# Kernel optimization log

Hardware: AMD Instinct MI355X
Metric: run time of the kernel (lower is better)

## Reference

```python
import jax, jax.numpy as jnp
import numpy as np

B, T, D = 256, 128, 1024
H = 128          # lstm_hidden
CF = 128         # conv_filters
K = 9            # num_labels
CE_W = 0.2
EPS = 1e-5


def conv1d(x, w, b, pad):
    # x: (B, C, T), w: (O, I, k)
    y = jax.lax.conv_general_dilated(x, w, (1,), [(pad, pad)],
                                     dimension_numbers=('NCH', 'OIH', 'NCH'))
    return y + b[None, :, None]


def batchnorm(x, g, beta):
    # training-mode BN over (N, W) per channel, biased variance (torch default)
    m = x.mean(axis=(0, 2), keepdims=True)
    v = x.var(axis=(0, 2), keepdims=True)
    return (x - m) * jax.lax.rsqrt(v + EPS) * g[None, :, None] + beta[None, :, None]


def lstm_dir(x, Wih, Whh, bih, bhh, reverse):
    # x: (B, T, D_in). PyTorch gate order: i, f, g, o.
    xg = jnp.einsum('btd,gd->btg', x, Wih) + bih + bhh  # (B, T, 4H)
    h0 = jnp.zeros((x.shape[0], Whh.shape[1]), x.dtype)
    c0 = jnp.zeros_like(h0)

    def step(carry, g_t):
        h, c = carry
        gates = g_t + h @ Whh.T
        i, f, g, o = jnp.split(gates, 4, axis=-1)
        c = jax.nn.sigmoid(f) * c + jax.nn.sigmoid(i) * jnp.tanh(g)
        h = jax.nn.sigmoid(o) * jnp.tanh(c)
        return (h, c), h

    _, hs = jax.lax.scan(step, (h0, c0), jnp.swapaxes(xg, 0, 1), reverse=reverse)
    return jnp.swapaxes(hs, 0, 1)  # (B, T, H)


def crf_log_partition(em, mask, start, trans, end):
    # em: (B, T, K), mask: (B, T) bool (mask[:,0] assumed True)
    score = start[None, :] + em[:, 0]  # (B, K)

    def step(score, inp):
        em_t, m_t = inp  # (B, K), (B,)
        nxt = jax.nn.logsumexp(score[:, :, None] + trans[None] + em_t[:, None, :], axis=1)
        return jnp.where(m_t[:, None], nxt, score), None

    score, _ = jax.lax.scan(step, score,
                            (jnp.swapaxes(em[:, 1:], 0, 1), jnp.swapaxes(mask[:, 1:], 0, 1)))
    return jax.nn.logsumexp(score + end[None, :], axis=1)  # (B,)


def crf_numerator(em, tags, mask, start, trans, end):
    mf = mask.astype(em.dtype)
    em_sc = jnp.take_along_axis(em, tags[..., None], axis=-1)[..., 0]  # (B, T)
    tr_sc = trans[tags[:, :-1], tags[:, 1:]]                           # (B, T-1)
    seq_ends = mask.astype(jnp.int32).sum(axis=1) - 1
    last_tags = jnp.take_along_axis(tags, seq_ends[:, None], axis=1)[:, 0]
    return (start[tags[:, 0]] + em_sc[:, 0]
            + ((tr_sc + em_sc[:, 1:]) * mf[:, 1:]).sum(axis=1)
            + end[last_tags])


def setup_inputs() -> dict:
    key = jax.random.key(0)
    ks = jax.random.split(key, 32)
    s = 0.05
    inp = {
        'embeddings': jax.random.normal(ks[0], (B, T, D), jnp.float32),
        'attention_mask': jnp.ones((B, T), jnp.int32),
        'labels': jax.random.randint(ks[1], (B, T), 0, K).astype(jnp.int64),
        'conv5_w': jax.random.normal(ks[2], (CF, D, 5)) * s,
        'conv5_b': jnp.zeros((CF,)),
        'bn1_g': jnp.ones((CF,)),
        'bn1_b': jnp.zeros((CF,)),
        'Wih_f': jax.random.normal(ks[3], (4 * H, CF)) * s,
        'Whh_f': jax.random.normal(ks[4], (4 * H, H)) * s,
        'bih_f': jnp.zeros((4 * H,)),
        'bhh_f': jnp.zeros((4 * H,)),
        'Wih_b': jax.random.normal(ks[5], (4 * H, CF)) * s,
        'Whh_b': jax.random.normal(ks[6], (4 * H, H)) * s,
        'bih_b': jnp.zeros((4 * H,)),
        'bhh_b': jnp.zeros((4 * H,)),
        'conv7_w': jax.random.normal(ks[7], (CF, 2 * H, 7)) * s,
        'conv7_b': jnp.zeros((CF,)),
        'conv9_w': jax.random.normal(ks[8], (CF, 2 * H, 9)) * s,
        'conv9_b': jnp.zeros((CF,)),
        'bn2_g': jnp.ones((2 * CF,)),
        'bn2_b': jnp.zeros((2 * CF,)),
        'cls_w': jax.random.normal(ks[9], (K, 2 * CF)) * s,
        'cls_b': jnp.zeros((K,)),
        'crf_start': jax.random.normal(ks[10], (K,)) * 0.1,
        'crf_trans': jax.random.normal(ks[11], (K, K)) * 0.1,
        'crf_end': jax.random.normal(ks[12], (K,)) * 0.1,
        'class_weights': jax.random.uniform(ks[13], (K,)) + 0.5,
    }
    return inp


def reference(embeddings, attention_mask, labels, conv5_w, conv5_b, bn1_g, bn1_b,
              Wih_f, Whh_f, bih_f, bhh_f, Wih_b, Whh_b, bih_b, bhh_b,
              conv7_w, conv7_b, conv9_w, conv9_b, bn2_g, bn2_b, cls_w, cls_b,
              crf_start, crf_trans, crf_end, class_weights):
    x = embeddings.astype(jnp.float32)
    xt = jnp.swapaxes(x, 1, 2)  # (B, D, T)
    xc = jax.nn.gelu(batchnorm(conv1d(xt, conv5_w, conv5_b, 2), bn1_g, bn1_b),
                     approximate=False)
    xl = jnp.swapaxes(xc, 1, 2)  # (B, T, CF)
    hf = lstm_dir(xl, Wih_f, Whh_f, bih_f, bhh_f, reverse=False)
    hb = lstm_dir(xl, Wih_b, Whh_b, bih_b, bhh_b, reverse=True)
    lstm_out = jnp.swapaxes(jnp.concatenate([hf, hb], axis=-1), 1, 2)  # (B, 2H, T)
    c7 = conv1d(lstm_out, conv7_w, conv7_b, 3)
    c9 = conv1d(lstm_out, conv9_w, conv9_b, 4)
    feat = jax.nn.gelu(batchnorm(jnp.concatenate([c7, c9], axis=1), bn2_g, bn2_b),
                       approximate=False)
    feat = jnp.swapaxes(feat, 1, 2)  # (B, T, 2CF); dropout p=0 -> identity
    logits = jnp.einsum('btf,kf->btk', feat, cls_w) + cls_b  # (B, T, K)

    mask = (attention_mask != 0) & (labels != -100)
    mod_labels = jnp.where(labels == -100, 0, labels).astype(jnp.int32)

    num = crf_numerator(logits, mod_labels, mask, crf_start, crf_trans, crf_end)
    logZ = crf_log_partition(logits, mask, crf_start, crf_trans, crf_end)
    crf_loss = -(num - logZ).mean()

    logp = jax.nn.log_softmax(logits, axis=-1).reshape(-1, K)
    y = labels.reshape(-1)
    valid = y != -100
    yi = jnp.where(valid, y, 0).astype(jnp.int32)
    nll = -jnp.take_along_axis(logp, yi[:, None], axis=1)[:, 0]
    w = jnp.where(valid, class_weights[yi], 0.0)
    ce_loss = (w * nll).sum() / w.sum()

    return (1.0 - CE_W) * crf_loss + CE_W * ce_loss
```

## Files before the change

kernel.cpp:

```cpp
#include <hip/hip_runtime.h>
#include <hip/hip_bf16.h>
#include <math.h>

#define BB 256
#define TT 128
#define DD 1024
#define CFF 128
#define HH 128
#define G4 512
#define NK 9

typedef __attribute__((ext_vector_type(8))) short bf16x8;
typedef __attribute__((ext_vector_type(4))) float f32x4;

__device__ __forceinline__ float bf_lo(unsigned u){ union{unsigned u; float f;} v; v.u = u << 16; return v.f; }
__device__ __forceinline__ float bf_hi(unsigned u){ union{unsigned u; float f;} v; v.u = u & 0xffff0000u; return v.f; }
__device__ __forceinline__ unsigned f2bf(float x){
    union{float f; unsigned u;} v; v.f = x;
    unsigned r = v.u + 0x7fffu + ((v.u >> 16) & 1u);
    return r >> 16;
}
__device__ __forceinline__ float fsig_fast(float x){
    return __builtin_amdgcn_rcpf(1.0f + __builtin_amdgcn_exp2f(-1.44269504f * x));
}
__device__ __forceinline__ float ftanh_fast(float x){
    return 1.0f - 2.0f * __builtin_amdgcn_rcpf(1.0f + __builtin_amdgcn_exp2f(2.88539008f * x));
}
__device__ __forceinline__ float gelu_exact(float x){
    return 0.5f*x*(1.0f + erff(x*0.70710678118654752440f));
}

__global__ __launch_bounds__(256) void prep_convw_kernel(
    const float* __restrict__ w, ushort* __restrict__ Wk, int CIN, int KS, int total)
{
    int i = blockIdx.x*256 + threadIdx.x;
    if (i >= total) return;
    int k = i % KS;
    int d = (i / KS) % CIN;
    int f = i / (KS * CIN);
    Wk[((size_t)(k*128 + f))*CIN + d] = (ushort)f2bf(w[i]);
}

__global__ __launch_bounds__(256) void prep_xg_kernel(
    const float* __restrict__ Wf, const float* __restrict__ Wb,
    const float* __restrict__ bif, const float* __restrict__ bhf,
    const float* __restrict__ bib, const float* __restrict__ bhb,
    ushort* __restrict__ Wxg, float* __restrict__ bias_xg)
{
    int i = blockIdx.x*256 + threadIdx.x;
    if (i < 65536) Wxg[i] = (ushort)f2bf(Wf[i]);
    else if (i < 131072) Wxg[i] = (ushort)f2bf(Wb[i - 65536]);
    else {
        int j = i - 131072;
        if (j < 512) bias_xg[j] = bif[j] + bhf[j];
        else if (j < 1024) bias_xg[j] = bib[j-512] + bhb[j-512];
    }
}

template<int CIN, int KS, int KSE_MAX, int SPLIT, bool IN_F32, bool OUT_BF16, bool XGT = false>
__global__ __launch_bounds__(256, 1) void conv_mfma_kernel(
    const void* __restrict__ in_v,
    const ushort* __restrict__ Wk_g,
    const float* __restrict__ bias_g,
    void* __restrict__ outA_v, void* __restrict__ outB_v,
    int OS, int co)
{
    constexpr int PAD = KS / 2;
    constexpr int ROWS = 128 + 2 * PAD;
    constexpr int NSTEP = (SPLIT == 1) ? (CIN / 64) : (CIN / 32);
    constexpr int ATOT = IN_F32 ? ROWS * 8 : ROWS * 4;
    constexpr int BTOT = KSE_MAX * 128 * 4;
    constexpr int AIT = (ATOT + 255) / 256;
    constexpr int BIT = (BTOT + 255) / 256;

    __shared__ ushort A_lds[ROWS * 32];
    __shared__ ushort B_lds[KSE_MAX * 128 * 32];

    const int tid = threadIdx.x;
    const int b   = blockIdx.x;
    const int by  = blockIdx.y;
    const int z   = blockIdx.z;
    const int dbase = (SPLIT == 1) ? z * (CIN / 2) : 0;
    const int k0    = (SPLIT == 2) ? z * KSE_MAX : 0;
    const int kse   = (SPLIT == 2) ? ((z == 0) ? KSE_MAX : (KS - KSE_MAX)) : KS;
    const ushort* __restrict__ Wk = Wk_g + (size_t)by * (size_t)(128 * CIN);
    const float* __restrict__ bias = bias_g + by * 128;

    float4 aRf[AIT];
    int4   aRb[AIT];
    int4   bR[BIT];

    auto stage_load = [&](int s) {
        const int d0 = dbase + s * 32;
        if constexpr (IN_F32) {
            const float* __restrict__ inp = (const float*)in_v;
#pragma unroll
            for (int it = 0; it < AIT; ++it) {
                int i = tid + it * 256;
                float4 v = make_float4(0.f, 0.f, 0.f, 0.f);
                if (i < ATOT) {
                    int r = i >> 3, c = i & 7;
                    int t = r - PAD;
                    if (t >= 0 && t < TT)
                        v = *reinterpret_cast<const float4*>(&inp[((size_t)b * TT + t) * CIN + d0 + c * 4]);
                }
                aRf[it] = v;
            }
        } else {
            const ushort* __restrict__ inp = (const ushort*)in_v;
#pragma unroll
            for (int it = 0; it < AIT; ++it) {
                int i = tid + it * 256;
                int4 v = make_int4(0, 0, 0, 0);
                if (i < ATOT) {
                    int r = i >> 2, c = i & 3;
                    int t = r - PAD;
                    if (t >= 0 && t < TT)
                        v = *reinterpret_cast<const int4*>(&inp[((size_t)b * TT + t) * CIN + d0 + c * 8]);
                }
                aRb[it] = v;
            }
        }
#pragma unroll
        for (int it = 0; it < BIT; ++it) {
            int i = tid + it * 256;
            int kk = i >> 9;
            int rem = i & 511;
            int f = rem >> 2, c = rem & 3;
            int4 v = make_int4(0, 0, 0, 0);
            if (kk < kse)
                v = *reinterpret_cast<const int4*>(&Wk[((size_t)((k0 + kk) * 128 + f)) * CIN + d0 + c * 8]);
            bR[it] = v;
        }
    };

    auto stage_write = [&]() {
        if constexpr (IN_F32) {
#pragma unroll
            for (int it = 0; it < AIT; ++it) {
                int i = tid + it * 256;
                if (i < ATOT) {
                    int r = i >> 3, c = i & 7;
                    float4 v = aRf[it];
                    ushort4 h;
                    h.x = (ushort)f2bf(v.x); h.y = (ushort)f2bf(v.y);
                    h.z = (ushort)f2bf(v.z); h.w = (ushort)f2bf(v.w);
                    int slot = (c >> 1) ^ (r & 3);
                    *reinterpret_cast<ushort4*>(&A_lds[r * 32 + slot * 8 + (c & 1) * 4]) = h;
                }
            }
        } else {
#pragma unroll
            for (int it = 0; it < AIT; ++it) {
                int i = tid + it * 256;
                if (i < ATOT) {
                    int r = i >> 2, c = i & 3;
                    int slot = c ^ (r & 3);
                    *reinterpret_cast<int4*>(&A_lds[r * 32 + slot * 8]) = aRb[it];
                }
            }
        }
#pragma unroll
        for (int it = 0; it < BIT; ++it) {
            int i = tid + it * 256;
            int kk = i >> 9;
            int rem = i & 511;
            int f = rem >> 2, c = rem & 3;
            int slot = c ^ (f & 3);
            *reinterpret_cast<int4*>(&B_lds[(kk * 128 + f) * 32 + slot * 8]) = bR[it];
        }
    };

    const int lane = tid & 63;
    const int wave = tid >> 6;
    const int lr = lane & 15;
    const int lk = lane >> 4;
    const int wm = wave >> 1;
    const int wn = wave & 1;

    f32x4 acc[4][4];
#pragma unroll
    for (int m = 0; m < 4; ++m)
#pragma unroll
        for (int n = 0; n < 4; ++n)
            acc[m][n] = (f32x4){0.f, 0.f, 0.f, 0.f};

    stage_load(0);
    stage_write();
    asm volatile("s_waitcnt lgkmcnt(0)" ::: "memory");
    __builtin_amdgcn_s_barrier();
    __builtin_amdgcn_sched_barrier(0);

    for (int s = 0; s < NSTEP; ++s) {
        if (s + 1 < NSTEP) stage_load(s + 1);
#pragma unroll
        for (int kk = 0; kk < KSE_MAX; ++kk) {
            bf16x8 af[4], bfr[4];
#pragma unroll
            for (int m = 0; m < 4; ++m) {
                int R = wm * 64 + m * 16 + lr + k0 + kk;
                if (kk >= kse) R = 0;
                af[m] = *reinterpret_cast<const bf16x8*>(&A_lds[R * 32 + ((lk ^ (R & 3)) * 8)]);
            }
#pragma unroll
            for (int n = 0; n < 4; ++n) {
                int Rb = kk * 128 + wn * 64 + n * 16 + lr;
                bfr[n] = *reinterpret_cast<const bf16x8*>(&B_lds[Rb * 32 + ((lk ^ (lr & 3)) * 8)]);
            }
#pragma unroll
            for (int m = 0; m < 4; ++m)
#pragma unroll
                for (int n = 0; n < 4; ++n)
                    acc[m][n] = __builtin_amdgcn_mfma_f32_16x16x32_bf16(af[m], bfr[n], acc[m][n], 0, 0, 0);
        }
        if (s + 1 < NSTEP) {
            asm volatile("s_waitcnt lgkmcnt(0)" ::: "memory");
            __builtin_amdgcn_s_barrier();
            __builtin_amdgcn_sched_barrier(0);
            stage_write();
            asm volatile("s_waitcnt lgkmcnt(0)" ::: "memory");
            __builtin_amdgcn_s_barrier();
            __builtin_amdgcn_sched_barrier(0);
        }
    }

    const bool addb = (SPLIT == 0) || (z == 0);
    void* out_v = (SPLIT != 0 && z == 1) ? outB_v : outA_v;
    float bv[4];
#pragma unroll
    for (int n = 0; n < 4; ++n) bv[n] = addb ? bias[wn * 64 + n * 16 + lr] : 0.f;
#pragma unroll
    for (int m = 0; m < 4; ++m) {
#pragma unroll
        for (int n = 0; n < 4; ++n) {
            int f = wn * 64 + n * 16 + lr;
#pragma unroll
            for (int q = 0; q < 4; ++q) {
                int trow = wm * 64 + m * 16 + lk * 4 + q;
                float val = acc[m][n][q] + bv[n];
                size_t idx;
                if constexpr (XGT) {
                    int dirg = by >> 2;
                    int g = by & 3;
                    idx = (size_t)dirg * 16777216u + (size_t)trow * 131072u
                        + (size_t)b * 512u + (size_t)(g * 128 + f);
                } else {
                    idx = ((size_t)b * TT + trow) * (size_t)OS + co + f;
                }
                if constexpr (OUT_BF16)
                    ((ushort*)out_v)[idx] = (ushort)f2bf(val);
                else
                    ((float*)out_v)[idx] = val;
            }
        }
    }
}

__global__ __launch_bounds__(256) void bn_stats_kernel(
    const float* __restrict__ y, const float* __restrict__ y2, int C, int rows_per_blk,
    float* __restrict__ sum, float* __restrict__ sqsum)
{
    int tpc = 256 / C;
    int c = threadIdx.x & (C - 1);
    int sub = threadIdx.x / C;
    size_t r0 = (size_t)blockIdx.x * rows_per_blk;
    float s = 0.f, s2 = 0.f;
    for (int r = sub; r < rows_per_blk; r += tpc) {
        size_t i = (r0 + r)*C + c;
        float v = y[i] + y2[i];
        s += v; s2 += v*v;
    }
    __shared__ float ls[256], ls2[256];
    ls[threadIdx.x] = s; ls2[threadIdx.x] = s2;
    __syncthreads();
    if (sub == 0) {
        for (int k = 1; k < tpc; ++k) { s += ls[c + k*C]; s2 += ls2[c + k*C]; }
        atomicAdd(&sum[c], s);
        atomicAdd(&sqsum[c], s2);
    }
}

__global__ __launch_bounds__(256) void bn_gelu_kernel(
    float* __restrict__ y, const float* __restrict__ y2, int Cmask,
    const float* __restrict__ sum, const float* __restrict__ sqsum,
    const float* __restrict__ g, const float* __restrict__ beta, float inv_n)
{
    size_t i = (size_t)blockIdx.x*256 + threadIdx.x;
    int c = (int)(i & (size_t)Cmask);
    float m = sum[c] * inv_n;
    float var = fmaxf(sqsum[c]*inv_n - m*m, 0.f);
    float xv = (y[i] + y2[i] - m) * rsqrtf(var + 1e-5f) * g[c] + beta[c];
    y[i] = gelu_exact(xv);
}

__global__ __launch_bounds__(512, 1) void lstm_mfma_kernel(
    const ushort* __restrict__ xg2,
    const float* __restrict__ Whhf, const float* __restrict__ Whhb,
    ushort* __restrict__ hfb)
{
    const int tid = threadIdx.x;
    const int lane = tid & 63;
    const int w = tid >> 6;
    const int jc = lane & 15;
    const int kq = lane >> 4;
    const int dir = blockIdx.x >> 4;
    const int b0 = (blockIdx.x & 15) << 4;
    const float* __restrict__ Whh = dir ? Whhb : Whhf;

    bf16x8 Wf[4][4];
#pragma unroll
    for (int g = 0; g < 4; ++g) {
        const float* wr = &Whh[(size_t)((g << 7) + (w << 4) + jc) * HH + (kq << 3)];
#pragma unroll
        for (int s = 0; s < 4; ++s) {
            float4 v0 = *reinterpret_cast<const float4*>(wr + (s << 5));
            float4 v1 = *reinterpret_cast<const float4*>(wr + (s << 5) + 4);
            union { bf16x8 v; ushort u[8]; } pk;
            pk.u[0] = (ushort)f2bf(v0.x); pk.u[1] = (ushort)f2bf(v0.y);
            pk.u[2] = (ushort)f2bf(v0.z); pk.u[3] = (ushort)f2bf(v0.w);
            pk.u[4] = (ushort)f2bf(v1.x); pk.u[5] = (ushort)f2bf(v1.y);
            pk.u[6] = (ushort)f2bf(v1.z); pk.u[7] = (ushort)f2bf(v1.w);
            Wf[g][s] = pk.v;
        }
    }

    __shared__ ushort h_lds[2][16 * 136];
    for (int i = tid; i < 16 * 136; i += 512) h_lds[0][i] = 0;
    f32x4 creg = (f32x4){0.f, 0.f, 0.f, 0.f};

    const ushort* __restrict__ xb = xg2 + (size_t)dir * 16777216u
        + (size_t)(b0 + jc) * 512u + (size_t)((w << 4) + (kq << 2));

    uint2 xA[4], xB[4];
    {
        int tt0 = dir ? (TT - 1) : 0;
        int tt1 = dir ? (TT - 2) : 1;
#pragma unroll
        for (int g = 0; g < 4; ++g) {
            xA[g] = *reinterpret_cast<const uint2*>(xb + (size_t)tt0 * 131072u + (g << 7));
            xB[g] = *reinterpret_cast<const uint2*>(xb + (size_t)tt1 * 131072u + (g << 7));
        }
    }

    __syncthreads();

    int cur = 0;
    const int hrd = jc * 136 + (kq << 3);
    const int col0 = (w << 4) + (kq << 2);

    auto step = [&](int t, uint2 (&xr)[4]) {
        const int tt_c = dir ? (TT - 1 - t) : t;
        f32x4 acc[4];
#pragma unroll
        for (int g = 0; g < 4; ++g) {
            acc[g][0] = bf_lo(xr[g].x);
            acc[g][1] = bf_hi(xr[g].x);
            acc[g][2] = bf_lo(xr[g].y);
            acc[g][3] = bf_hi(xr[g].y);
        }
        {
            int t2 = t + 2; if (t2 >= TT) t2 = TT - 1;
            int ttn = dir ? (TT - 1 - t2) : t2;
#pragma unroll
            for (int g = 0; g < 4; ++g)
                xr[g] = *reinterpret_cast<const uint2*>(xb + (size_t)ttn * 131072u + (g << 7));
        }
        bf16x8 Hf[4];
#pragma unroll
        for (int s = 0; s < 4; ++s)
            Hf[s] = *reinterpret_cast<const bf16x8*>(&h_lds[cur][hrd + (s << 5)]);
#pragma unroll
        for (int s = 0; s < 4; ++s)
#pragma unroll
            for (int g = 0; g < 4; ++g)
                acc[g] = __builtin_amdgcn_mfma_f32_16x16x32_bf16(Wf[g][s], Hf[s], acc[g], 0, 0, 0);
        float hv[4];
#pragma unroll
        for (int r = 0; r < 4; ++r) {
            float iv = fsig_fast(acc[0][r]);
            float fv = fsig_fast(acc[1][r]);
            float gv = ftanh_fast(acc[2][r]);
            float ov = fsig_fast(acc[3][r]);
            float c = fv * creg[r] + iv * gv;
            creg[r] = c;
            hv[r] = ov * ftanh_fast(c);
        }
        ushort4 hb;
        hb.x = (ushort)f2bf(hv[0]); hb.y = (ushort)f2bf(hv[1]);
        hb.z = (ushort)f2bf(hv[2]); hb.w = (ushort)f2bf(hv[3]);
        const int nxt = cur ^ 1;
        *reinterpret_cast<ushort4*>(&h_lds[nxt][jc * 136 + col0]) = hb;
        *reinterpret_cast<ushort4*>(&hfb[((size_t)(b0 + jc) * TT + tt_c) * 256 + (dir << 7) + col0]) = hb;
        asm volatile("s_waitcnt lgkmcnt(0)" ::: "memory");
        __builtin_amdgcn_s_barrier();
        __builtin_amdgcn_sched_barrier(0);
        cur = nxt;
    };

    for (int t = 0; t < TT; t += 2) {
        step(t, xA);
        step(t + 1, xB);
    }
}

__global__ __launch_bounds__(256) void logits_kernel(
    const float* __restrict__ feat, const float* __restrict__ cw,
    const float* __restrict__ cb, float* __restrict__ lg)
{
    __shared__ float wls[NK*256];
    for (int i = threadIdx.x; i < NK*256; i += 256) wls[i] = cw[i];
    __syncthreads();
    size_t row = (size_t)blockIdx.x*256 + threadIdx.x;
    const float* fr = &feat[row*256];
    float acc[NK];
#pragma unroll
    for (int k = 0; k < NK; ++k) acc[k] = 0.f;
    for (int c = 0; c < 256; c += 4) {
        float4 v = *reinterpret_cast<const float4*>(&fr[c]);
#pragma unroll
        for (int k = 0; k < NK; ++k)
            acc[k] += v.x*wls[k*256 + c] + v.y*wls[k*256 + c + 1]
                    + v.z*wls[k*256 + c + 2] + v.w*wls[k*256 + c + 3];
    }
#pragma unroll
    for (int k = 0; k < NK; ++k) lg[row*NK + k] = acc[k] + cb[k];
}

__global__ __launch_bounds__(256) void ce_kernel(
    const float* __restrict__ lg, const int* __restrict__ labels,
    const float* __restrict__ cw, float* __restrict__ acc2)
{
    size_t i = (size_t)blockIdx.x*256 + threadIdx.x;
    const float* l = &lg[i*NK];
    float mx = -1e30f;
#pragma unroll
    for (int k = 0; k < NK; ++k) mx = fmaxf(mx, l[k]);
    float se = 0.f;
#pragma unroll
    for (int k = 0; k < NK; ++k) se += expf(l[k] - mx);
    float lz = mx + logf(se);
    int y = labels[i];
    bool valid = (y != -100);
    int yi = valid ? y : 0;
    float nll = lz - l[yi];
    float wv = valid ? cw[yi] : 0.f;
    __shared__ float s1[256], s2[256];
    s1[threadIdx.x] = wv*nll;
    s2[threadIdx.x] = wv;
    __syncthreads();
    for (int s = 128; s > 0; s >>= 1) {
        if (threadIdx.x < s) { s1[threadIdx.x] += s1[threadIdx.x + s]; s2[threadIdx.x] += s2[threadIdx.x + s]; }
        __syncthreads();
    }
    if (threadIdx.x == 0) { atomicAdd(&acc2[0], s1[0]); atomicAdd(&acc2[1], s2[0]); }
}

__global__ __launch_bounds__(64) void crf_kernel(
    const float* __restrict__ lg, const int* __restrict__ att,
    const int* __restrict__ labels, const float* __restrict__ startv,
    const float* __restrict__ trans, const float* __restrict__ endv,
    float* __restrict__ numo, float* __restrict__ logzo)
{
    int b = blockIdx.x;
    int lane = threadIdx.x;
    int lane_c = (lane < NK) ? lane : 0;
    const float* em = &lg[(size_t)b*TT*NK];
    float tr[NK];
#pragma unroll
    for (int i = 0; i < NK; ++i) tr[i] = trans[i*NK + lane_c];
    float score = startv[lane_c] + em[lane_c];

    for (int t = 1; t < TT; ++t) {
        int lt = labels[b*TT + t];
        bool m = (att[b*TT + t] != 0) && (lt != -100);
        float vals[NK];
#pragma unroll
        for (int i = 0; i < NK; ++i)
            vals[i] = __shfl(score, i, 64) + tr[i];
        if (m) {
            float mx = vals[0];
#pragma unroll
            for (int i = 1; i < NK; ++i) mx = fmaxf(mx, vals[i]);
            float sm = 0.f;
#pragma unroll
            for (int i = 0; i < NK; ++i) sm += expf(vals[i] - mx);
            score = mx + logf(sm) + em[t*NK + lane_c];
        }
    }
    float fin = (lane < NK) ? (score + endv[lane_c]) : -1e30f;
    float mx = -1e30f;
#pragma unroll
    for (int i = 0; i < NK; ++i) mx = fmaxf(mx, __shfl(fin, i, 64));
    float sm = 0.f;
#pragma unroll
    for (int i = 0; i < NK; ++i) sm += expf(__shfl(fin, i, 64) - mx);
    if (lane == 0) logzo[b] = mx + logf(sm);

    if (lane == 0) {
        int l0 = labels[b*TT];
        int tag0 = (l0 == -100) ? 0 : l0;
        bool m0 = (att[b*TT] != 0) && (l0 != -100);
        float num = startv[tag0] + em[tag0];
        int prev = tag0;
        int cnt = m0 ? 1 : 0;
        for (int t = 1; t < TT; ++t) {
            int lt = labels[b*TT + t];
            bool m = (att[b*TT + t] != 0) && (lt != -100);
            int tag = (lt == -100) ? 0 : lt;
            if (m) { num += trans[prev*NK + tag] + em[t*NK + tag]; cnt++; }
            prev = tag;
        }
        int le = cnt - 1; if (le < 0) le = 0; if (le >= TT) le = TT - 1;
        int ll = labels[b*TT + le];
        int ltag = (ll == -100) ? 0 : ll;
        num += endv[ltag];
        numo[b] = num;
    }
}

__global__ __launch_bounds__(256) void finalize_kernel(
    const float* __restrict__ numo, const float* __restrict__ logzo,
    const float* __restrict__ acc2, float* __restrict__ out)
{
    __shared__ float red[256];
    int tid = threadIdx.x;
    red[tid] = numo[tid] - logzo[tid];
    __syncthreads();
    for (int s = 128; s > 0; s >>= 1) {
        if (tid < s) red[tid] += red[tid + s];
        __syncthreads();
    }
    if (tid == 0) {
        float crf = -(red[0] / (float)BB);
        float ce = acc2[0] / acc2[1];
        out[0] = 0.8f*crf + 0.2f*ce;
    }
}

extern "C" void kernel_launch(void* const* d_in, const int* in_sizes, int n_in,
                              void* d_out, int out_size, void* d_ws, size_t ws_size,
                              hipStream_t stream)
{
    const float* emb   = (const float*)d_in[0];
    const int*   att   = (const int*)  d_in[1];
    const int*   lab   = (const int*)  d_in[2];
    const float* c5w   = (const float*)d_in[3];
    const float* c5b   = (const float*)d_in[4];
    const float* bn1g  = (const float*)d_in[5];
    const float* bn1b  = (const float*)d_in[6];
    const float* Wihf  = (const float*)d_in[7];
    const float* Whhf  = (const float*)d_in[8];
    const float* bihf  = (const float*)d_in[9];
    const float* bhhf  = (const float*)d_in[10];
    const float* Wihb  = (const float*)d_in[11];
    const float* Whhb  = (const float*)d_in[12];
    const float* bihb  = (const float*)d_in[13];
    const float* bhhb  = (const float*)d_in[14];
    const float* c7w   = (const float*)d_in[15];
    const float* c7b   = (const float*)d_in[16];
    const float* c9w   = (const float*)d_in[17];
    const float* c9b   = (const float*)d_in[18];
    const float* bn2g  = (const float*)d_in[19];
    const float* bn2b  = (const float*)d_in[20];
    const float* clsw  = (const float*)d_in[21];
    const float* clsb  = (const float*)d_in[22];
    const float* cstart= (const float*)d_in[23];
    const float* ctrans= (const float*)d_in[24];
    const float* cend  = (const float*)d_in[25];
    const float* cwts  = (const float*)d_in[26];
    (void)in_sizes; (void)n_in; (void)out_size; (void)ws_size;

    char* wsb = (char*)d_ws;
    size_t off = 0;
    auto alloc = [&](size_t bytes) { void* p = wsb + off; off += (bytes + 255) & ~(size_t)255; return p; };
    float*  y1      = (float*) alloc((size_t)4194304*4);
    ushort* xg      = (ushort*)alloc((size_t)2*16777216*2);
    ushort* hfb     = (ushort*)alloc((size_t)8388608*2);
    float*  lg      = (float*) alloc((size_t)294912*4);
    ushort* Wk5     = (ushort*)alloc((size_t)655360*2);
    ushort* Wk7     = (ushort*)alloc((size_t)229376*2);
    ushort* Wk9     = (ushort*)alloc((size_t)294912*2);
    ushort* Wxg     = (ushort*)alloc((size_t)131072*2);
    float*  bias_xg = (float*) alloc((size_t)1024*4);
    float*  stats   = (float*) alloc((size_t)2048*4);
    float* y1b  = (float*)xg;
    float* c79a = (float*)xg;
    float* c79b = (float*)(xg + 16777216);
    float* bn1s = stats;
    float* bn1q = stats + 128;
    float* bn2s = stats + 256;
    float* bn2q = stats + 512;
    float* acc2 = stats + 768;
    float* numo = stats + 770;
    float* logzo = numo + 256;

    hipMemsetAsync(stats, 0, 770*sizeof(float), stream);

    prep_convw_kernel<<<2560, 256, 0, stream>>>(c5w, Wk5, 1024, 5, 655360);
    prep_convw_kernel<<<896,  256, 0, stream>>>(c7w, Wk7, 256, 7, 229376);
    prep_convw_kernel<<<1152, 256, 0, stream>>>(c9w, Wk9, 256, 9, 294912);
    prep_xg_kernel<<<516, 256, 0, stream>>>(Wihf, Wihb, bihf, bhhf, bihb, bhhb, Wxg, bias_xg);

    conv_mfma_kernel<1024,5,5,1,true,false><<<dim3(256,1,2), 256, 0, stream>>>(emb, Wk5, c5b, y1, y1b, 128, 0);
    bn_stats_kernel<<<256, 256, 0, stream>>>(y1, y1b, 128, 128, bn1s, bn1q);
    bn_gelu_kernel<<<16384, 256, 0, stream>>>(y1, y1b, 127, bn1s, bn1q, bn1g, bn1b, 1.0f/32768.f);

    conv_mfma_kernel<128,1,1,0,true,true,true><<<dim3(256,8,1), 256, 0, stream>>>(y1, Wxg, bias_xg, xg, nullptr, 512, 0);
    lstm_mfma_kernel<<<32, 512, 0, stream>>>(xg, Whhf, Whhb, hfb);

    conv_mfma_kernel<256,7,4,2,false,false><<<dim3(256,1,2), 256, 0, stream>>>(hfb, Wk7, c7b, c79a, c79b, 256, 0);
    conv_mfma_kernel<256,9,5,2,false,false><<<dim3(256,1,2), 256, 0, stream>>>(hfb, Wk9, c9b, c79a, c79b, 256, 128);
    bn_stats_kernel<<<256, 256, 0, stream>>>(c79a, c79b, 256, 128, bn2s, bn2q);
    bn_gelu_kernel<<<32768, 256, 0, stream>>>(c79a, c79b, 255, bn2s, bn2q, bn2g, bn2b, 1.0f/32768.f);

    logits_kernel<<<128, 256, 0, stream>>>(c79a, clsw, clsb, lg);
    ce_kernel<<<128, 256, 0, stream>>>(lg, lab, cwts, acc2);
    crf_kernel<<<BB, 64, 0, stream>>>(lg, att, lab, cstart, ctrans, cend, numo, logzo);
    finalize_kernel<<<1, 256, 0, stream>>>(numo, logzo, acc2, (float*)d_out);
}
```

Before: 484.0 us.

## Fuse BN2+GELU into logits, emit bf16 from BN1, streamline LSTM step

```diff
diff --git a/kernel.cpp b/kernel.cpp
--- a/kernel.cpp
+++ b/kernel.cpp
@@ -280,17 +280,18 @@
     }
 }
 
-__global__ __launch_bounds__(256) void bn_gelu_kernel(
-    float* __restrict__ y, const float* __restrict__ y2, int Cmask,
+__global__ __launch_bounds__(256) void bn_gelu_bf16_kernel(
+    const float* __restrict__ y, const float* __restrict__ y2,
     const float* __restrict__ sum, const float* __restrict__ sqsum,
-    const float* __restrict__ g, const float* __restrict__ beta, float inv_n)
+    const float* __restrict__ g, const float* __restrict__ beta,
+    ushort* __restrict__ out, float inv_n)
 {
     size_t i = (size_t)blockIdx.x*256 + threadIdx.x;
-    int c = (int)(i & (size_t)Cmask);
+    int c = (int)(i & 127);
     float m = sum[c] * inv_n;
     float var = fmaxf(sqsum[c]*inv_n - m*m, 0.f);
     float xv = (y[i] + y2[i] - m) * rsqrtf(var + 1e-5f) * g[c] + beta[c];
-    y[i] = gelu_exact(xv);
+    out[i] = (ushort)f2bf(gelu_exact(xv));
 }
 
 __global__ __launch_bounds__(512, 1) void lstm_mfma_kernel(
@@ -328,28 +329,33 @@
     for (int i = tid; i < 16 * 136; i += 512) h_lds[0][i] = 0;
     f32x4 creg = (f32x4){0.f, 0.f, 0.f, 0.f};
 
-    const ushort* __restrict__ xb = xg2 + (size_t)dir * 16777216u
-        + (size_t)(b0 + jc) * 512u + (size_t)((w << 4) + (kq << 2));
+    const int col0 = (w << 4) + (kq << 2);
+    const int hrd = jc * 136 + (kq << 3);
+
+    const ptrdiff_t dstep = dir ? -131072 : 131072;
+    const int tt0 = dir ? (TT - 1) : 0;
+    const ushort* pA = xg2 + (size_t)dir * 16777216u + (size_t)(b0 + jc) * 512u
+                     + (size_t)col0 + (size_t)tt0 * 131072u;
+    const ushort* pB = pA + dstep;
 
     uint2 xA[4], xB[4];
-    {
-        int tt0 = dir ? (TT - 1) : 0;
-        int tt1 = dir ? (TT - 2) : 1;
-#pragma unroll
-        for (int g = 0; g < 4; ++g) {
-            xA[g] = *reinterpret_cast<const uint2*>(xb + (size_t)tt0 * 131072u + (g << 7));
-            xB[g] = *reinterpret_cast<const uint2*>(xb + (size_t)tt1 * 131072u + (g << 7));
-        }
-    }
+#pragma unroll
+    for (int g = 0; g < 4; ++g) {
+        xA[g] = *reinterpret_cast<const uint2*>(pA + (g << 7));
+        xB[g] = *reinterpret_cast<const uint2*>(pB + (g << 7));
+    }
+    pA += 2 * dstep;
+    pB += 2 * dstep;
+
+    ushort* hp = hfb + (size_t)(b0 + jc) * (TT * 256) + (size_t)tt0 * 256
+               + (dir << 7) + col0;
+    const ptrdiff_t hstep = dir ? -256 : 256;
 
     __syncthreads();
 
     int cur = 0;
-    const int hrd = jc * 136 + (kq << 3);
-    const int col0 = (w << 4) + (kq << 2);
-
-    auto step = [&](int t, uint2 (&xr)[4]) {
-        const int tt_c = dir ? (TT - 1 - t) : t;
+
+    auto step = [&](uint2 (&xr)[4], const ushort*& pp) {
         f32x4 acc[4];
 #pragma unroll
         for (int g = 0; g < 4; ++g) {
@@ -358,13 +364,10 @@
             acc[g][2] = bf_lo(xr[g].y);
             acc[g][3] = bf_hi(xr[g].y);
         }
-        {
-            int t2 = t + 2; if (t2 >= TT) t2 = TT - 1;
-            int ttn = dir ? (TT - 1 - t2) : t2;
-#pragma unroll
-            for (int g = 0; g < 4; ++g)
-                xr[g] = *reinterpret_cast<const uint2*>(xb + (size_t)ttn * 131072u + (g << 7));
-        }
+#pragma unroll
+        for (int g = 0; g < 4; ++g)
+            xr[g] = *reinterpret_cast<const uint2*>(pp + (g << 7));
+        pp += 2 * dstep;
         bf16x8 Hf[4];
 #pragma unroll
         for (int s = 0; s < 4; ++s)
@@ -385,42 +388,63 @@
             creg[r] = c;
             hv[r] = ov * ftanh_fast(c);
         }
-        ushort4 hb;
-        hb.x = (ushort)f2bf(hv[0]); hb.y = (ushort)f2bf(hv[1]);
-        hb.z = (ushort)f2bf(hv[2]); hb.w = (ushort)f2bf(hv[3]);
+        uint2 hb;
+        asm("v_cvt_pk_bf16_f32 %0, %1, %2" : "=v"(hb.x) : "v"(hv[0]), "v"(hv[1]));
+        asm("v_cvt_pk_bf16_f32 %0, %1, %2" : "=v"(hb.y) : "v"(hv[2]), "v"(hv[3]));
         const int nxt = cur ^ 1;
-        *reinterpret_cast<ushort4*>(&h_lds[nxt][jc * 136 + col0]) = hb;
-        *reinterpret_cast<ushort4*>(&hfb[((size_t)(b0 + jc) * TT + tt_c) * 256 + (dir << 7) + col0]) = hb;
+        *reinterpret_cast<uint2*>(&h_lds[nxt][jc * 136 + col0]) = hb;
         asm volatile("s_waitcnt lgkmcnt(0)" ::: "memory");
         __builtin_amdgcn_s_barrier();
         __builtin_amdgcn_sched_barrier(0);
+        *reinterpret_cast<uint2*>(hp) = hb;
+        hp += hstep;
         cur = nxt;
     };
 
     for (int t = 0; t < TT; t += 2) {
-        step(t, xA);
-        step(t + 1, xB);
-    }
-}
-
-__global__ __launch_bounds__(256) void logits_kernel(
-    const float* __restrict__ feat, const float* __restrict__ cw,
-    const float* __restrict__ cb, float* __restrict__ lg)
+        step(xA, pA);
+        step(xB, pB);
+    }
+}
+
+__global__ __launch_bounds__(256) void logits_bn_kernel(
+    const float* __restrict__ a, const float* __restrict__ bpart,
+    const float* __restrict__ sum, const float* __restrict__ sqsum,
+    const float* __restrict__ g, const float* __restrict__ beta,
+    const float* __restrict__ cw, const float* __restrict__ cb,
+    float* __restrict__ lg, float inv_n)
 {
     __shared__ float wls[NK*256];
+    __shared__ float sc_lds[256], sh_lds[256];
     for (int i = threadIdx.x; i < NK*256; i += 256) wls[i] = cw[i];
+    {
+        int c = threadIdx.x;
+        float m = sum[c] * inv_n;
+        float var = fmaxf(sqsum[c]*inv_n - m*m, 0.f);
+        float rs = rsqrtf(var + 1e-5f);
+        float s = rs * g[c];
+        sc_lds[c] = s;
+        sh_lds[c] = beta[c] - m * s;
+    }
     __syncthreads();
     size_t row = (size_t)blockIdx.x*256 + threadIdx.x;
-    const float* fr = &feat[row*256];
+    const float* ar = &a[row*256];
+    const float* br = &bpart[row*256];
     float acc[NK];
 #pragma unroll
     for (int k = 0; k < NK; ++k) acc[k] = 0.f;
     for (int c = 0; c < 256; c += 4) {
-        float4 v = *reinterpret_cast<const float4*>(&fr[c]);
-#pragma unroll
-        for (int k = 0; k < NK; ++k)
-            acc[k] += v.x*wls[k*256 + c] + v.y*wls[k*256 + c + 1]
-                    + v.z*wls[k*256 + c + 2] + v.w*wls[k*256 + c + 3];
+        float4 av = *reinterpret_cast<const float4*>(&ar[c]);
+        float4 bv = *reinterpret_cast<const float4*>(&br[c]);
+        float vv[4] = {av.x + bv.x, av.y + bv.y, av.z + bv.z, av.w + bv.w};
+#pragma unroll
+        for (int j = 0; j < 4; ++j) {
+            float xv = vv[j] * sc_lds[c + j] + sh_lds[c + j];
+            float f = gelu_exact(xv);
+#pragma unroll
+            for (int k = 0; k < NK; ++k)
+                acc[k] += f * wls[k*256 + c + j];
+        }
     }
 #pragma unroll
     for (int k = 0; k < NK; ++k) lg[row*NK + k] = acc[k] + cb[k];
@@ -576,6 +600,7 @@
     float*  y1      = (float*) alloc((size_t)4194304*4);
     ushort* xg      = (ushort*)alloc((size_t)2*16777216*2);
     ushort* hfb     = (ushort*)alloc((size_t)8388608*2);
+    ushort* y1h     = (ushort*)alloc((size_t)4194304*2);
     float*  lg      = (float*) alloc((size_t)294912*4);
     ushort* Wk5     = (ushort*)alloc((size_t)655360*2);
     ushort* Wk7     = (ushort*)alloc((size_t)229376*2);
@@ -603,17 +628,16 @@
 
     conv_mfma_kernel<1024,5,5,1,true,false><<<dim3(256,1,2), 256, 0, stream>>>(emb, Wk5, c5b, y1, y1b, 128, 0);
     bn_stats_kernel<<<256, 256, 0, stream>>>(y1, y1b, 128, 128, bn1s, bn1q);
-    bn_gelu_kernel<<<16384, 256, 0, stream>>>(y1, y1b, 127, bn1s, bn1q, bn1g, bn1b, 1.0f/32768.f);
-
-    conv_mfma_kernel<128,1,1,0,true,true,true><<<dim3(256,8,1), 256, 0, stream>>>(y1, Wxg, bias_xg, xg, nullptr, 512, 0);
+    bn_gelu_bf16_kernel<<<16384, 256, 0, stream>>>(y1, y1b, bn1s, bn1q, bn1g, bn1b, y1h, 1.0f/32768.f);
+
+    conv_mfma_kernel<128,1,1,0,false,true,true><<<dim3(256,8,1), 256, 0, stream>>>(y1h, Wxg, bias_xg, xg, nullptr, 512, 0);
     lstm_mfma_kernel<<<32, 512, 0, stream>>>(xg, Whhf, Whhb, hfb);
 
     conv_mfma_kernel<256,7,4,2,false,false><<<dim3(256,1,2), 256, 0, stream>>>(hfb, Wk7, c7b, c79a, c79b, 256, 0);
     conv_mfma_kernel<256,9,5,2,false,false><<<dim3(256,1,2), 256, 0, stream>>>(hfb, Wk9, c9b, c79a, c79b, 256, 128);
     bn_stats_kernel<<<256, 256, 0, stream>>>(c79a, c79b, 256, 128, bn2s, bn2q);
-    bn_gelu_kernel<<<32768, 256, 0, stream>>>(c79a, c79b, 255, bn2s, bn2q, bn2g, bn2b, 1.0f/32768.f);
-
-    logits_kernel<<<128, 256, 0, stream>>>(c79a, clsw, clsb, lg);
+
+    logits_bn_kernel<<<128, 256, 0, stream>>>(c79a, c79b, bn2s, bn2q, bn2g, bn2b, clsw, clsb, lg, 1.0f/32768.f);
     ce_kernel<<<128, 256, 0, stream>>>(lg, lab, cwts, acc2);
     crf_kernel<<<BB, 64, 0, stream>>>(lg, att, lab, cstart, ctrans, cend, numo, logzo);
     finalize_kernel<<<1, 256, 0, stream>>>(numo, logzo, acc2, (float*)d_out);
```

Result: slower. 494.2 us (+2.1%).
